# Kernel tuning notes

Measured on AMD Instinct MI355X. Metric: run time of the kernel, lower is better.

The kernel has to match this reference:

```python
import jax, jax.numpy as jnp
import numpy as np

B, N, C, H, W = 2, 2048, 1024, 16, 8  # batch, seq, dim, heads, band half-width
HD = C // H
SCALE = HD ** -0.5


def band_mask(n, w):
    # rows i: allowed cols lo..hi inclusive, matching get_attn_mask
    i = jnp.arange(n)[:, None]
    j = jnp.arange(n)[None, :]
    lo = jnp.where(i <= w, 0, i - w)
    hi = jnp.where(n - i <= w, n - 1, i + w)
    return (j >= lo) & (j <= hi)  # [N, N] bool


def setup_inputs() -> dict:
    key = jax.random.key(0)
    k1, k2, k3 = jax.random.split(key, 3)
    x = jax.random.normal(k1, (B, N, C), dtype=jnp.float32)
    Wqkv = jax.random.normal(k2, (C, 3 * C), dtype=jnp.float32) * (C ** -0.5)
    Wproj = jax.random.normal(k3, (C, C), dtype=jnp.float32) * (C ** -0.5)
    bproj = jnp.zeros((C,), dtype=jnp.float32)
    return {"x": x, "Wqkv": Wqkv, "Wproj": Wproj, "bproj": bproj}


def reference(x, Wqkv, Wproj, bproj):
    b, n, c = x.shape
    qkv = (x @ Wqkv).reshape(b, n, 3, H, HD)
    qkv = jnp.transpose(qkv, (2, 0, 3, 1, 4))  # [3, B, H, N, HD]
    q, k, v = qkv[0], qkv[1], qkv[2]
    attn = jnp.einsum('bhqd,bhkd->bhqk', q, k) * SCALE
    mask = band_mask(n, W)  # [N, N]
    attn = jnp.where(mask[None, None], attn, jnp.float32(-1e9))
    attn = jax.nn.softmax(attn, axis=-1)
    # dropout omitted (eval mode / deterministic reference)
    out = jnp.einsum('bhqk,bhkd->bhqd', attn, v)
    out = jnp.transpose(out, (0, 2, 1, 3)).reshape(b, n, c)
    return out @ Wproj + bproj
```

## Files before the change

kernel.cpp:

```cpp
#include <hip/hip_runtime.h>

typedef unsigned short ushort_t;
typedef unsigned int uint32;

typedef __bf16 bf16x8 __attribute__((ext_vector_type(8)));
typedef float f32x16 __attribute__((ext_vector_type(16)));

__device__ __forceinline__ uint32 f2bf1(float f) {
  uint32 b = __float_as_uint(f);
  return (b + 0x7FFFu + ((b >> 16) & 1u)) >> 16;
}
__device__ __forceinline__ uint32 packbf2(float a, float b) {
  return f2bf1(a) | (f2bf1(b) << 16);
}
__device__ __forceinline__ float bflo(uint32 u) { return __uint_as_float(u << 16); }
__device__ __forceinline__ float bfhi(uint32 u) { return __uint_as_float(u & 0xFFFF0000u); }

__device__ __forceinline__ void gload16(const void* g, void* l) {
  __builtin_amdgcn_global_load_lds(
      (const __attribute__((address_space(1))) unsigned int*)g,
      (__attribute__((address_space(3))) unsigned int*)l, 16, 0, 0);
}

__global__ __launch_bounds__(256) void prep_inputs(
    const float* __restrict__ x, ushort_t* __restrict__ xb,
    const float* __restrict__ Wqkv, ushort_t* __restrict__ wqkvT,
    const float* __restrict__ Wproj, ushort_t* __restrict__ wprT) {
  int bx = blockIdx.x;
  const int tid = threadIdx.x;
  if (bx < 4096) {
    const int i = bx * 256 + tid;
    float4 v = ((const float4*)x)[i];
    uint2 r;
    r.x = packbf2(v.x, v.y);
    r.y = packbf2(v.z, v.w);
    ((uint2*)xb)[i] = r;
    return;
  }
  bx -= 4096;
  const int gx = bx & 127, gy = bx >> 7;
  __shared__ float tile[32][33];
  const int tx = tid & 31, ty = tid >> 5;
  const float* src;
  ushort_t* dst;
  int Cc, c0;
  if (gx < 96) { src = Wqkv;  dst = wqkvT; Cc = 3072; c0 = gx << 5; }
  else         { src = Wproj; dst = wprT;  Cc = 1024; c0 = (gx - 96) << 5; }
  const int r0 = gy << 5;
#pragma unroll
  for (int i = 0; i < 4; ++i)
    tile[ty + i * 8][tx] = src[(size_t)(r0 + ty + i * 8) * Cc + c0 + tx];
  __syncthreads();
#pragma unroll
  for (int i = 0; i < 4; ++i)
    dst[(size_t)(c0 + ty + i * 8) * 1024 + r0 + tx] = (ushort_t)f2bf1(tile[tx][ty + i * 8]);
}


template <int ROWS>
__device__ __forceinline__ void stage2(ushort_t* dst, const ushort_t* gbase,
                                       int ldK, int tid) {
  const int r = tid >> 2, s = tid & 3;
  const int c = ((s ^ ((r >> 1) & 3)) << 3);
  const int wvb = (tid >> 6) << 9;
  const ushort_t* g = gbase + (size_t)r * ldK + c;
  gload16(g, dst + wvb);
  if (ROWS == 128) gload16(g + (size_t)64 * ldK, dst + 2048 + wvb);
}

template <bool OUT_BF16, int MF2, int NF2>
__global__ __launch_bounds__(256) void gemm2p(
    const ushort_t* __restrict__ A, const ushort_t* __restrict__ Bt,
    void* __restrict__ Cout, const float* __restrict__ bias,
    const int M, const int Nn, const int K) {
  constexpr int BM = MF2 * 64, BN = NF2 * 64;
  constexpr int AL = BM * 32, BL = BN * 32;
  __shared__ ushort_t lA[2 * AL];
  __shared__ ushort_t lB[2 * BL];
  const int tid = threadIdx.x;
  const int lane = tid & 63, wave = tid >> 6;
  const int wm = wave >> 1, wn = wave & 1;
  const int bm = blockIdx.y * BM, bn = blockIdx.x * BN;

  const int r31 = lane & 31, h = lane >> 5;
  const int sw = (r31 >> 1) & 3;
  const int c0 = ((h ^ sw) << 3);
  const int c1 = (((2 + h) ^ sw) << 3);

  const ushort_t* gA = A + (size_t)bm * K;
  const ushort_t* gB = Bt + (size_t)bn * K;

  f32x16 acc[MF2][NF2] = {};

  stage2<BM>(lA, gA, K, tid);
  stage2<BN>(lB, gB, K, tid);
  __syncthreads();

  int buf = 0;
  for (int k0 = 0; k0 < K; k0 += 32) {
    if (k0 + 32 < K) {
      stage2<BM>(lA + (buf ^ 1) * AL, gA + k0 + 32, K, tid);
      stage2<BN>(lB + (buf ^ 1) * BL, gB + k0 + 32, K, tid);
    }
    bf16x8 a[MF2][2], b[NF2][2];
#pragma unroll
    for (int m = 0; m < MF2; ++m) {
      const int rowA = buf * AL + ((wm * MF2 + m) * 32 + r31) * 32;
      a[m][0] = *(const bf16x8*)&lA[rowA + c0];
      a[m][1] = *(const bf16x8*)&lA[rowA + c1];
    }
#pragma unroll
    for (int n = 0; n < NF2; ++n) {
      const int rowB = buf * BL + ((wn * NF2 + n) * 32 + r31) * 32;
      b[n][0] = *(const bf16x8*)&lB[rowB + c0];
      b[n][1] = *(const bf16x8*)&lB[rowB + c1];
    }
#pragma unroll
    for (int ks = 0; ks < 2; ++ks)
#pragma unroll
      for (int m = 0; m < MF2; ++m)
#pragma unroll
        for (int n = 0; n < NF2; ++n)
          acc[m][n] = __builtin_amdgcn_mfma_f32_32x32x16_bf16(
              a[m][ks], b[n][ks], acc[m][n], 0, 0, 0);
    __syncthreads();
    buf ^= 1;
  }

  const int rb = bm + wm * (MF2 * 32) + 4 * h;
  const int cb = bn + wn * (NF2 * 32) + r31;
#pragma unroll
  for (int m = 0; m < MF2; ++m)
#pragma unroll
    for (int n = 0; n < NF2; ++n)
#pragma unroll
      for (int reg = 0; reg < 16; ++reg) {
        const int row = rb + m * 32 + (reg & 3) + 8 * (reg >> 2);
        const int col = cb + n * 32;
        if (OUT_BF16)
          ((ushort_t*)Cout)[(size_t)row * Nn + col] = (ushort_t)f2bf1(acc[m][n][reg]);
        else
          ((float*)Cout)[(size_t)row * Nn + col] = acc[m][n][reg] + bias[col];
      }
}

__global__ __launch_bounds__(256) void attn_band(
    const ushort_t* __restrict__ qkv, ushort_t* __restrict__ aout) {
  __shared__ float Ks[80 * 68];
  __shared__ float Vs[80 * 68];
  const int tid = threadIdx.x;
  const int i0 = blockIdx.x << 6;
  const int h = blockIdx.y;
  const int b = blockIdx.z;
  const size_t rowbase = (size_t)b * 2048;

  for (int idx = tid; idx < 1280; idx += 256) {
    const int t = idx >> 4, c = idx & 15;
    const int j = i0 - 8 + t;
    float k0 = 0.f, k1 = 0.f, k2 = 0.f, k3 = 0.f;
    float v0 = 0.f, v1 = 0.f, v2 = 0.f, v3 = 0.f;
    if ((unsigned)j < 2048u) {
      const ushort_t* p = qkv + (rowbase + j) * 3072 + (h << 6) + (c << 2);
      uint2 rk = *(const uint2*)(p + 1024);
      uint2 rv = *(const uint2*)(p + 2048);
      k0 = bflo(rk.x); k1 = bfhi(rk.x); k2 = bflo(rk.y); k3 = bfhi(rk.y);
      v0 = bflo(rv.x); v1 = bfhi(rv.x); v2 = bflo(rv.y); v3 = bfhi(rv.y);
    }
    *(float4*)&Ks[t * 68 + (c << 2)] = make_float4(k0, k1, k2, k3);
    *(float4*)&Vs[t * 68 + (c << 2)] = make_float4(v0, v1, v2, v3);
  }
  __syncthreads();

  const int lane = tid & 63, wv = tid >> 6;
  const int qs = lane >> 2, dg = lane & 3;
  const int qi = (wv << 4) + qs;
  const int i = i0 + qi;

  const ushort_t* qp = qkv + (rowbase + i) * 3072 + (h << 6) + (dg << 4);
  float q[16];
  {
    uint4 u0 = *(const uint4*)qp;
    uint4 u1 = *(const uint4*)(qp + 8);
    q[0] = bflo(u0.x); q[1] = bfhi(u0.x); q[2] = bflo(u0.y); q[3] = bfhi(u0.y);
    q[4] = bflo(u0.z); q[5] = bfhi(u0.z); q[6] = bflo(u0.w); q[7] = bfhi(u0.w);
    q[8] = bflo(u1.x); q[9] = bfhi(u1.x); q[10] = bflo(u1.y); q[11] = bfhi(u1.y);
    q[12] = bflo(u1.z); q[13] = bfhi(u1.z); q[14] = bflo(u1.w); q[15] = bfhi(u1.w);
  }

  float s[17];
#pragma unroll
  for (int jo = 0; jo < 17; ++jo) {
    const float* kr = &Ks[(qi + jo) * 68 + (dg << 4)];
    float d = 0.f;
#pragma unroll
    for (int c = 0; c < 4; ++c) {
      float4 kv = *(const float4*)(kr + (c << 2));
      d += q[c * 4 + 0] * kv.x + q[c * 4 + 1] * kv.y +
           q[c * 4 + 2] * kv.z + q[c * 4 + 3] * kv.w;
    }
    d += __shfl_xor(d, 1);
    d += __shfl_xor(d, 2);
    const int jg = i - 8 + jo;
    s[jo] = ((unsigned)jg < 2048u) ? d * 0.125f : -1e30f;
  }
  float m = s[0];
#pragma unroll
  for (int jo = 1; jo < 17; ++jo) m = fmaxf(m, s[jo]);
  float sum = 0.f;
#pragma unroll
  for (int jo = 0; jo < 17; ++jo) {
    s[jo] = __expf(s[jo] - m);
    sum += s[jo];
  }
  const float inv = 1.f / sum;

  float o[16];
#pragma unroll
  for (int dd = 0; dd < 16; ++dd) o[dd] = 0.f;
#pragma unroll
  for (int jo = 0; jo < 17; ++jo) {
    const float* vr = &Vs[(qi + jo) * 68 + (dg << 4)];
    const float w = s[jo];
#pragma unroll
    for (int c = 0; c < 4; ++c) {
      float4 vv = *(const float4*)(vr + (c << 2));
      o[c * 4 + 0] += w * vv.x; o[c * 4 + 1] += w * vv.y;
      o[c * 4 + 2] += w * vv.z; o[c * 4 + 3] += w * vv.w;
    }
  }

  ushort_t* op = aout + (rowbase + i) * 1024 + (h << 6) + (dg << 4);
  uint4 w0, w1;
  w0.x = packbf2(o[0] * inv, o[1] * inv);
  w0.y = packbf2(o[2] * inv, o[3] * inv);
  w0.z = packbf2(o[4] * inv, o[5] * inv);
  w0.w = packbf2(o[6] * inv, o[7] * inv);
  w1.x = packbf2(o[8] * inv, o[9] * inv);
  w1.y = packbf2(o[10] * inv, o[11] * inv);
  w1.z = packbf2(o[12] * inv, o[13] * inv);
  w1.w = packbf2(o[14] * inv, o[15] * inv);
  *(uint4*)op = w0;
  *(uint4*)(op + 8) = w1;
}

extern "C" void kernel_launch(void* const* d_in, const int* in_sizes, int n_in,
                              void* d_out, int out_size, void* d_ws, size_t ws_size,
                              hipStream_t stream) {
  const float* x = (const float*)d_in[0];
  const float* Wqkv = (const float*)d_in[1];
  const float* Wproj = (const float*)d_in[2];
  const float* bproj = (const float*)d_in[3];
  float* out = (float*)d_out;

  char* ws = (char*)d_ws;
  ushort_t* xb    = (ushort_t*)(ws);
  ushort_t* wqkvT = (ushort_t*)(ws + (8u << 20));
  ushort_t* wprT  = (ushort_t*)(ws + (14u << 20));
  ushort_t* qkv   = (ushort_t*)(ws + (16u << 20));
  ushort_t* aoutb = (ushort_t*)(ws + (40u << 20));

  prep_inputs<<<8192, 256, 0, stream>>>(x, xb, Wqkv, wqkvT, Wproj, wprT);
  gemm2p<true, 2, 2><<<dim3(24, 32), 256, 0, stream>>>(
      xb, wqkvT, qkv, nullptr, 4096, 3072, 1024);
  attn_band<<<dim3(32, 16, 2), 256, 0, stream>>>(qkv, aoutb);
  gemm2p<false, 1, 2><<<dim3(8, 64), 256, 0, stream>>>(
      aoutb, wprT, out, bproj, 4096, 1024, 1024);
}
```

Measured before the change: 84.61 us.

## Triple-buffer GEMM LDS staging with partial vmcnt waits instead of full syncthreads

```diff
diff --git a/kernel.cpp b/kernel.cpp
--- a/kernel.cpp
+++ b/kernel.cpp
@@ -20,6 +20,20 @@
   __builtin_amdgcn_global_load_lds(
       (const __attribute__((address_space(1))) unsigned int*)g,
       (__attribute__((address_space(3))) unsigned int*)l, 16, 0, 0);
+}
+
+__device__ __forceinline__ bf16x8 dsr16(unsigned byteaddr) {
+  bf16x8 r;
+  asm volatile("ds_read_b128 %0, %1" : "=v"(r) : "v"(byteaddr));
+  return r;
+}
+
+template <int N>
+__device__ __forceinline__ void vmcnt_wait() {
+  if constexpr (N == 0) asm volatile("s_waitcnt vmcnt(0)");
+  else if constexpr (N == 3) asm volatile("s_waitcnt vmcnt(3)");
+  else if constexpr (N == 4) asm volatile("s_waitcnt vmcnt(4)");
+  else static_assert(N == 0 || N == 3 || N == 4, "unsupported vmcnt");
 }
 
 __global__ __launch_bounds__(256) void prep_inputs(
@@ -69,14 +83,16 @@
 }
 
 template <bool OUT_BF16, int MF2, int NF2>
-__global__ __launch_bounds__(256) void gemm2p(
+__global__ __launch_bounds__(256) void gemm3p(
     const ushort_t* __restrict__ A, const ushort_t* __restrict__ Bt,
     void* __restrict__ Cout, const float* __restrict__ bias,
     const int M, const int Nn, const int K) {
   constexpr int BM = MF2 * 64, BN = NF2 * 64;
   constexpr int AL = BM * 32, BL = BN * 32;
-  __shared__ ushort_t lA[2 * AL];
-  __shared__ ushort_t lB[2 * BL];
+  constexpr unsigned ALb = AL * 2, BLb = BL * 2;
+  constexpr int LP = (BM == 128 ? 2 : 1) + (BN == 128 ? 2 : 1);
+  __shared__ ushort_t lA[3 * AL];
+  __shared__ ushort_t lB[3 * BL];
   const int tid = threadIdx.x;
   const int lane = tid & 63, wave = tid >> 6;
   const int wm = wave >> 1, wn = wave & 1;
@@ -84,8 +100,10 @@
 
   const int r31 = lane & 31, h = lane >> 5;
   const int sw = (r31 >> 1) & 3;
-  const int c0 = ((h ^ sw) << 3);
-  const int c1 = (((2 + h) ^ sw) << 3);
+  const unsigned c0b = ((h ^ sw) << 3) * 2;
+  const unsigned c1b = (((2 + h) ^ sw) << 3) * 2;
+  const unsigned lbA = (unsigned)(uintptr_t)&lA[0];
+  const unsigned lbB = (unsigned)(uintptr_t)&lB[0];
 
   const ushort_t* gA = A + (size_t)bm * K;
   const ushort_t* gB = Bt + (size_t)bn * K;
@@ -94,27 +112,36 @@
 
   stage2<BM>(lA, gA, K, tid);
   stage2<BN>(lB, gB, K, tid);
-  __syncthreads();
-
-  int buf = 0;
+  stage2<BM>(lA + AL, gA + 32, K, tid);
+  stage2<BN>(lB + BL, gB + 32, K, tid);
+  vmcnt_wait<LP>();
+  __builtin_amdgcn_s_barrier();
+
+  unsigned curA = lbA, curB = lbB;
+  ushort_t* stA = lA + 2 * AL;
+  ushort_t* stB = lB + 2 * BL;
+
   for (int k0 = 0; k0 < K; k0 += 32) {
-    if (k0 + 32 < K) {
-      stage2<BM>(lA + (buf ^ 1) * AL, gA + k0 + 32, K, tid);
-      stage2<BN>(lB + (buf ^ 1) * BL, gB + k0 + 32, K, tid);
+    const bool s2 = (k0 + 64) < K;
+    if (s2) {
+      stage2<BM>(stA, gA + k0 + 64, K, tid);
+      stage2<BN>(stB, gB + k0 + 64, K, tid);
     }
     bf16x8 a[MF2][2], b[NF2][2];
 #pragma unroll
     for (int m = 0; m < MF2; ++m) {
-      const int rowA = buf * AL + ((wm * MF2 + m) * 32 + r31) * 32;
-      a[m][0] = *(const bf16x8*)&lA[rowA + c0];
-      a[m][1] = *(const bf16x8*)&lA[rowA + c1];
+      const unsigned rA = curA + (unsigned)(((wm * MF2 + m) * 32 + r31) * 64);
+      a[m][0] = dsr16(rA + c0b);
+      a[m][1] = dsr16(rA + c1b);
     }
 #pragma unroll
     for (int n = 0; n < NF2; ++n) {
-      const int rowB = buf * BL + ((wn * NF2 + n) * 32 + r31) * 32;
-      b[n][0] = *(const bf16x8*)&lB[rowB + c0];
-      b[n][1] = *(const bf16x8*)&lB[rowB + c1];
-    }
+      const unsigned rB = curB + (unsigned)(((wn * NF2 + n) * 32 + r31) * 64);
+      b[n][0] = dsr16(rB + c0b);
+      b[n][1] = dsr16(rB + c1b);
+    }
+    asm volatile("s_waitcnt lgkmcnt(0)");
+    __builtin_amdgcn_sched_barrier(0);
 #pragma unroll
     for (int ks = 0; ks < 2; ++ks)
 #pragma unroll
@@ -123,8 +150,12 @@
         for (int n = 0; n < NF2; ++n)
           acc[m][n] = __builtin_amdgcn_mfma_f32_32x32x16_bf16(
               a[m][ks], b[n][ks], acc[m][n], 0, 0, 0);
-    __syncthreads();
-    buf ^= 1;
+    if (s2) vmcnt_wait<LP>(); else vmcnt_wait<0>();
+    __builtin_amdgcn_s_barrier();
+    curA += ALb; if (curA == lbA + 3 * ALb) curA = lbA;
+    curB += BLb; if (curB == lbB + 3 * BLb) curB = lbB;
+    stA += AL; if (stA == lA + 3 * AL) stA = lA;
+    stB += BL; if (stB == lB + 3 * BL) stB = lB;
   }
 
   const int rb = bm + wm * (MF2 * 32) + 4 * h;
@@ -260,9 +291,9 @@
   ushort_t* aoutb = (ushort_t*)(ws + (40u << 20));
 
   prep_inputs<<<8192, 256, 0, stream>>>(x, xb, Wqkv, wqkvT, Wproj, wprT);
-  gemm2p<true, 2, 2><<<dim3(24, 32), 256, 0, stream>>>(
+  gemm3p<true, 2, 2><<<dim3(24, 32), 256, 0, stream>>>(
       xb, wqkvT, qkv, nullptr, 4096, 3072, 1024);
   attn_band<<<dim3(32, 16, 2), 256, 0, stream>>>(qkv, aoutb);
-  gemm2p<false, 1, 2><<<dim3(8, 64), 256, 0, stream>>>(
+  gemm3p<false, 1, 2><<<dim3(8, 64), 256, 0, stream>>>(
       aoutb, wprT, out, bproj, 4096, 1024, 1024);
 }
```

Result: no change. 84.08 us (-0.6%).
